# Performance work log

Measured on AMD Instinct MI355X. Metric: run time of the kernel, lower is better.

Reference implementation:

```python
import jax, jax.numpy as jnp
import numpy as np


def setup_inputs() -> dict:
    key = jax.random.key(0)
    ks = jax.random.split(key, 6)
    B, T, U = 4, 160, 80
    De, Dd = 640, 640
    inner, vocab = 640, 1024
    return {
        "enc_state": jax.random.normal(ks[0], (B, T, De), jnp.float32),
        "dec_state": jax.random.normal(ks[1], (B, U, Dd), jnp.float32),
        "W1": jax.random.normal(ks[2], (De + Dd, inner), jnp.float32) * (1.0 / np.sqrt(De + Dd)),
        "b1": jax.random.normal(ks[3], (inner,), jnp.float32) * 0.02,
        "W2": jax.random.normal(ks[4], (inner, vocab), jnp.float32) * (1.0 / np.sqrt(inner)),
        "b2": jax.random.normal(ks[5], (vocab,), jnp.float32) * 0.02,
    }


def reference(enc_state, dec_state, W1, b1, W2, b2):
    # Faithful to: cat([enc tiled over U, dec tiled over T], -1) @ W1 + b1,
    # algebraically split so the [B,T,U,2D] concat is never materialized:
    # cat(e, d) @ W1 == e @ W1[:De] + d @ W1[De:]
    De = enc_state.shape[-1]
    W1_enc, W1_dec = W1[:De], W1[De:]
    enc_proj = jnp.einsum("btd,dh->bth", enc_state, W1_enc)   # [B,T,H]
    dec_proj = jnp.einsum("bud,dh->buh", dec_state, W1_dec)   # [B,U,H]
    # broadcast add over the (T,U) lattice -> [B,T,U,H]
    hidden = jnp.tanh(enc_proj[:, :, None, :] + dec_proj[:, None, :, :] + b1)
    logits = jnp.einsum("btuh,hv->btuv", hidden, W2) + b2     # [B,T,U,V]
    return logits
```

## Files before the change

### kernel.cpp

```cpp
#include <hip/hip_runtime.h>
#include <hip/hip_bf16.h>
#include <cstdint>

#define B_    4
#define T_    160
#define U_    80
#define D_    640
#define V_    1024
#define BT_   640
#define BU_   320
#define M_    51200

typedef __bf16 bf16x8 __attribute__((ext_vector_type(8)));
typedef float floatx4 __attribute__((ext_vector_type(4)));

__device__ __forceinline__ void g2l16(const void* g, void* l) {
    __builtin_amdgcn_global_load_lds((const __attribute__((address_space(1))) void*)g,
                                     (__attribute__((address_space(3))) void*)l,
                                     16, 0, 0);
}

__device__ __forceinline__ float fast_tanh(float x) {
    float e = __builtin_amdgcn_exp2f(x * 2.8853900817779268f);
    return 1.0f - 2.0f * __builtin_amdgcn_rcpf(e + 1.0f);
}

__global__ __launch_bounds__(256) void proj_kernel(
    const float* __restrict__ enc, const float* __restrict__ dec,
    const float* __restrict__ W1,
    float* __restrict__ encp, float* __restrict__ decp) {
    __shared__ float As[32][36];
    __shared__ float Ws[32][36];

    const int rt = blockIdx.y;
    const int ct = blockIdx.x;
    const float* Asrc;
    const float* Wsrc;
    float* Cdst;
    if (rt < 20) { Asrc = enc + (size_t)rt * 32 * D_;        Wsrc = W1;             Cdst = encp + (size_t)rt * 32 * D_; }
    else         { Asrc = dec + (size_t)(rt - 20) * 32 * D_; Wsrc = W1 + D_ * D_;   Cdst = decp + (size_t)(rt - 20) * 32 * D_; }

    const int tid = threadIdx.x;
    const int ar = tid >> 3, ac = (tid & 7) * 4;
    const int tr = tid >> 4, tc = tid & 15;

    float a00 = 0.f, a01 = 0.f, a10 = 0.f, a11 = 0.f;
    for (int k0 = 0; k0 < D_; k0 += 32) {
        __syncthreads();
        *(floatx4*)&As[ar][ac] = *(const floatx4*)&Asrc[(size_t)ar * D_ + k0 + ac];
        *(floatx4*)&Ws[ar][ac] = *(const floatx4*)&Wsrc[(size_t)(k0 + ar) * D_ + ct * 32 + ac];
        __syncthreads();
#pragma unroll
        for (int kk = 0; kk < 32; kk++) {
            float x0 = As[tr * 2][kk], x1 = As[tr * 2 + 1][kk];
            float w0 = Ws[kk][tc * 2], w1 = Ws[kk][tc * 2 + 1];
            a00 += x0 * w0; a01 += x0 * w1;
            a10 += x1 * w0; a11 += x1 * w1;
        }
    }
    const int cc = ct * 32 + tc * 2;
    Cdst[(size_t)(tr * 2) * D_ + cc]     = a00;
    Cdst[(size_t)(tr * 2) * D_ + cc + 1] = a01;
    Cdst[(size_t)(tr * 2 + 1) * D_ + cc]     = a10;
    Cdst[(size_t)(tr * 2 + 1) * D_ + cc + 1] = a11;
}

__global__ __launch_bounds__(256) void w2t_kernel(
    const float* __restrict__ W2, __bf16* __restrict__ W2t) {
    __shared__ __bf16 tile[32][33];
    const int vt = blockIdx.x;
    const int kt = blockIdx.y;
    const int tx = threadIdx.x & 31, ty = threadIdx.x >> 5;
#pragma unroll
    for (int i = 0; i < 4; i++)
        tile[ty + i * 8][tx] = (__bf16)W2[(size_t)(kt * 32 + ty + i * 8) * V_ + vt * 32 + tx];
    __syncthreads();
#pragma unroll
    for (int i = 0; i < 4; i++)
        W2t[(size_t)(vt * 32 + ty + i * 8) * D_ + kt * 32 + tx] = tile[tx][ty + i * 8];
}

__global__ __launch_bounds__(256) void hidden_kernel(
    const float* __restrict__ encp, const float* __restrict__ decp,
    const float* __restrict__ b1, __bf16* __restrict__ H) {
    const unsigned g = blockIdx.x * 256u + threadIdx.x;
    const unsigned row = g / 80u;
    const unsigned hg  = g % 80u;
    const unsigned u   = row % 80u;
    const unsigned bt  = row / 80u;
    const unsigned b   = bt / 160u;

    const float* ep = encp + (size_t)bt * D_ + hg * 8;
    const float* dp = decp + (size_t)(b * 80u + u) * D_ + hg * 8;
    const float* bp = b1 + hg * 8;

    floatx4 e0 = *(const floatx4*)ep,       e1 = *(const floatx4*)(ep + 4);
    floatx4 d0 = *(const floatx4*)dp,       d1 = *(const floatx4*)(dp + 4);
    floatx4 c0 = *(const floatx4*)bp,       c1 = *(const floatx4*)(bp + 4);

    bf16x8 hv;
#pragma unroll
    for (int i = 0; i < 4; i++) hv[i]     = (__bf16)fast_tanh(e0[i] + d0[i] + c0[i]);
#pragma unroll
    for (int i = 0; i < 4; i++) hv[i + 4] = (__bf16)fast_tanh(e1[i] + d1[i] + c1[i]);

    *(bf16x8*)(H + (size_t)g * 8) = hv;
}

#define VM4  asm volatile("s_waitcnt vmcnt(4)" ::: "memory")
#define VM0  asm volatile("s_waitcnt vmcnt(0)" ::: "memory")
#define BAR  __builtin_amdgcn_s_barrier()
#define SCB  __builtin_amdgcn_sched_barrier(0)

#define STG_A(BUF, S, TL) do { \
    g2l16(Hb + (unsigned)((S)*163840 + (TL)*128) + agl,         ldsp + (BUF)*32768 + (S)*16384 + stl); \
    g2l16(Hb + (unsigned)((S)*163840 + (TL)*128 + 10240) + agl, ldsp + (BUF)*32768 + (S)*16384 + stl + 1024); \
  } while (0)
#define STG_B(BUF, S, TL) do { \
    g2l16(Wb + (unsigned)((S)*163840 + (TL)*128) + agl,         ldsp + 65536 + (BUF)*32768 + (S)*16384 + stl); \
    g2l16(Wb + (unsigned)((S)*163840 + (TL)*128 + 10240) + agl, ldsp + 65536 + (BUF)*32768 + (S)*16384 + stl + 1024); \
  } while (0)

#define PHASE(QM, QN, ABUF, BBUF, STAGE_STMT, WAIT_STMT) do { \
    bf16x8 af0[4], af1[4], bg0[2], bg1[2]; \
    _Pragma("unroll") for (int ii = 0; ii < 4; ++ii) { \
      af0[ii] = *(const bf16x8*)(ldsp + (ABUF)*32768 + (QM)*16384 + ii*2048 + aRowB + sx0); \
      af1[ii] = *(const bf16x8*)(ldsp + (ABUF)*32768 + (QM)*16384 + ii*2048 + aRowB + sx1); \
    } \
    _Pragma("unroll") for (int jj = 0; jj < 2; ++jj) { \
      bg0[jj] = *(const bf16x8*)(ldsp + 65536 + (BBUF)*32768 + (QN)*16384 + jj*2048 + bRowB + sx0); \
      bg1[jj] = *(const bf16x8*)(ldsp + 65536 + (BBUF)*32768 + (QN)*16384 + jj*2048 + bRowB + sx1); \
    } \
    STAGE_STMT; \
    WAIT_STMT; \
    BAR; SCB; \
    __builtin_amdgcn_s_setprio(1); \
    _Pragma("unroll") for (int ii = 0; ii < 4; ++ii) \
      _Pragma("unroll") for (int jj = 0; jj < 2; ++jj) { \
        acc[(QM)*4+ii][(QN)*2+jj] = __builtin_amdgcn_mfma_f32_16x16x32_bf16(af0[ii], bg0[jj], acc[(QM)*4+ii][(QN)*2+jj], 0, 0, 0); \
        acc[(QM)*4+ii][(QN)*2+jj] = __builtin_amdgcn_mfma_f32_16x16x32_bf16(af1[ii], bg1[jj], acc[(QM)*4+ii][(QN)*2+jj], 0, 0, 0); \
      } \
    __builtin_amdgcn_s_setprio(0); \
    BAR; SCB; \
  } while (0)

__global__ __launch_bounds__(512, 2) void gemm_kernel(
    const __bf16* __restrict__ H, const __bf16* __restrict__ W2t,
    const float* __restrict__ b2, float* __restrict__ C) {
    __shared__ __align__(128) char lds[131072];

    const int bid = blockIdx.x;
    const int swz = (bid & 7) * 100 + (bid >> 3);
    const int mt = swz >> 2, nt = swz & 3;
    const int m0 = mt * 256, n0 = nt * 256;

    const int tid = threadIdx.x;
    const int w = tid >> 6, l = tid & 63;
    const int wr = w >> 2, wc = w & 3;
    const int lrow = l & 15, lk = l >> 4, l7 = l & 7, lhi = l >> 3;

    const unsigned swzb = (unsigned)(((l & 7) ^ lhi) * 16);
    const unsigned agl  = (unsigned)((w * 16 + lhi) * 1280) + swzb;
    const unsigned stl  = (unsigned)(w * 2048 + l * 16);

    const char* Hb = (const char*)H   + (size_t)m0 * 1280;
    const char* Wb = (const char*)W2t + (size_t)n0 * 1280;
    char* ldsp = (char*)lds;

    const unsigned aRowB = (unsigned)((wr * 64 + lrow) * 128);
    const unsigned bRowB = (unsigned)(wc * 4096 + lrow * 128);
    const unsigned sx0 = (unsigned)(((0 + lk) ^ l7) * 16);
    const unsigned sx1 = (unsigned)(((4 + lk) ^ l7) * 16);

    floatx4 acc[8][4] = {};

    STG_A(0, 0, 0); STG_A(0, 1, 0); STG_B(0, 0, 0); STG_B(0, 1, 0);
    STG_A(1, 0, 1); STG_B(1, 0, 1);
    VM4; BAR; SCB;

#pragma unroll 1
    for (int it = 0; it < 5; ++it) {
        const int t1 = 2 * it + 1, t2 = 2 * it + 2, t3 = 2 * it + 3;
        const bool pf = (it < 4);
        PHASE(0, 0, 0, 0, { STG_A(1, 1, t1); STG_B(1, 1, t1); }, (void)0);
        PHASE(0, 1, 0, 0, (void)0, (void)0);
        PHASE(1, 0, 0, 0, { if (pf) STG_A(0, 0, t2); }, (void)0);
        PHASE(1, 1, 0, 0, { if (pf) STG_B(0, 0, t2); },
                          { if (it == 4) { VM0; } else { VM4; } });
        PHASE(0, 0, 1, 1, { if (pf) { STG_A(0, 1, t2); STG_B(0, 1, t2); } }, (void)0);
        PHASE(0, 1, 1, 1, (void)0, (void)0);
        PHASE(1, 0, 1, 1, { if (pf) STG_A(1, 0, t3); }, (void)0);
        PHASE(1, 1, 1, 1, { if (pf) STG_B(1, 0, t3); }, VM4);
    }

#pragma unroll
    for (int j = 0; j < 4; ++j) {
        const int col = n0 + (j >> 1) * 128 + wc * 32 + (j & 1) * 16 + lrow;
        const float bj = b2[col];
#pragma unroll
        for (int i = 0; i < 8; ++i) {
            const int row = m0 + (i >> 2) * 128 + wr * 64 + (i & 3) * 16 + lk * 4;
            float* Cp = C + (size_t)row * V_ + col;
#pragma unroll
            for (int rg = 0; rg < 4; ++rg)
                Cp[(size_t)rg * V_] = acc[i][j][rg] + bj;
        }
    }
}

extern "C" void kernel_launch(void* const* d_in, const int* in_sizes, int n_in,
                              void* d_out, int out_size, void* d_ws, size_t ws_size,
                              hipStream_t stream) {
    const float* enc = (const float*)d_in[0];
    const float* dec = (const float*)d_in[1];
    const float* W1  = (const float*)d_in[2];
    const float* b1  = (const float*)d_in[3];
    const float* W2  = (const float*)d_in[4];
    const float* b2  = (const float*)d_in[5];
    float* out = (float*)d_out;

    char* ws = (char*)d_ws;
    float*  encp = (float*)ws;
    float*  decp = (float*)(ws + 1638400);
    __bf16* W2t  = (__bf16*)(ws + 1638400 + 819200);
    __bf16* Hbuf = (__bf16*)(ws + 1638400 + 819200 + 1310720);

    proj_kernel<<<dim3(20, 30), 256, 0, stream>>>(enc, dec, W1, encp, decp);
    w2t_kernel<<<dim3(32, 20), 256, 0, stream>>>(W2, W2t);
    hidden_kernel<<<16000, 256, 0, stream>>>(encp, decp, b1, Hbuf);
    gemm_kernel<<<800, 512, 0, stream>>>(Hbuf, W2t, b2, out);
}
```

Baseline: 345.3 us.

## Reuse MFMA fragments across GEMM phases and enlarge projection tiles

The bf16 GEMM main loop now reads A and B fragments from LDS once and reuses them across neighbouring quadrant phases. A fragments are shared across the two N-quadrants and B fragments across the two M-quadrants, which cuts LDS read traffic per K-step. The fp32 projection kernel moves from 32x32 tiles with 2x2 per-thread outputs to 64x64 tiles with 4x4 register blocking and vectorised stores, raising arithmetic intensity. The cost is more live fragment registers in the GEMM, which could pressure occupancy at 512 threads and 2 blocks per CU. The projection launch also shrinks to 150 blocks, which may underfill the GPU.

```diff
diff --git a/kernel.cpp b/kernel.cpp
--- a/kernel.cpp
+++ b/kernel.cpp
@@ -29,40 +29,45 @@
     const float* __restrict__ enc, const float* __restrict__ dec,
     const float* __restrict__ W1,
     float* __restrict__ encp, float* __restrict__ decp) {
-    __shared__ float As[32][36];
-    __shared__ float Ws[32][36];
+    __shared__ float As[64][36];
+    __shared__ float Ws[32][68];
 
     const int rt = blockIdx.y;
     const int ct = blockIdx.x;
-    const float* Asrc;
-    const float* Wsrc;
-    float* Cdst;
-    if (rt < 20) { Asrc = enc + (size_t)rt * 32 * D_;        Wsrc = W1;             Cdst = encp + (size_t)rt * 32 * D_; }
-    else         { Asrc = dec + (size_t)(rt - 20) * 32 * D_; Wsrc = W1 + D_ * D_;   Cdst = decp + (size_t)(rt - 20) * 32 * D_; }
+    const float* Asrc; const float* Wsrc; float* Cdst;
+    if (rt < 10) { Asrc = enc + (size_t)rt * 64 * D_;        Wsrc = W1;           Cdst = encp + (size_t)rt * 64 * D_; }
+    else         { Asrc = dec + (size_t)(rt - 10) * 64 * D_; Wsrc = W1 + D_ * D_; Cdst = decp + (size_t)(rt - 10) * 64 * D_; }
 
     const int tid = threadIdx.x;
-    const int ar = tid >> 3, ac = (tid & 7) * 4;
-    const int tr = tid >> 4, tc = tid & 15;
-
-    float a00 = 0.f, a01 = 0.f, a10 = 0.f, a11 = 0.f;
+    const int ar = tid >> 2,  ac = (tid & 3) * 8;
+    const int wr2 = tid >> 3, wc2 = (tid & 7) * 8;
+    const int tr = tid >> 4,  tc = tid & 15;
+
+    float acc[4][4] = {};
     for (int k0 = 0; k0 < D_; k0 += 32) {
         __syncthreads();
-        *(floatx4*)&As[ar][ac] = *(const floatx4*)&Asrc[(size_t)ar * D_ + k0 + ac];
-        *(floatx4*)&Ws[ar][ac] = *(const floatx4*)&Wsrc[(size_t)(k0 + ar) * D_ + ct * 32 + ac];
+        *(floatx4*)&As[ar][ac]       = *(const floatx4*)&Asrc[(size_t)ar * D_ + k0 + ac];
+        *(floatx4*)&As[ar][ac + 4]   = *(const floatx4*)&Asrc[(size_t)ar * D_ + k0 + ac + 4];
+        *(floatx4*)&Ws[wr2][wc2]     = *(const floatx4*)&Wsrc[(size_t)(k0 + wr2) * D_ + ct * 64 + wc2];
+        *(floatx4*)&Ws[wr2][wc2 + 4] = *(const floatx4*)&Wsrc[(size_t)(k0 + wr2) * D_ + ct * 64 + wc2 + 4];
         __syncthreads();
 #pragma unroll
         for (int kk = 0; kk < 32; kk++) {
-            float x0 = As[tr * 2][kk], x1 = As[tr * 2 + 1][kk];
-            float w0 = Ws[kk][tc * 2], w1 = Ws[kk][tc * 2 + 1];
-            a00 += x0 * w0; a01 += x0 * w1;
-            a10 += x1 * w0; a11 += x1 * w1;
+            floatx4 w = *(const floatx4*)&Ws[kk][tc * 4];
+            float a0 = As[tr * 4 + 0][kk], a1 = As[tr * 4 + 1][kk];
+            float a2 = As[tr * 4 + 2][kk], a3 = As[tr * 4 + 3][kk];
+#pragma unroll
+            for (int j = 0; j < 4; j++) {
+                acc[0][j] += a0 * w[j]; acc[1][j] += a1 * w[j];
+                acc[2][j] += a2 * w[j]; acc[3][j] += a3 * w[j];
+            }
         }
     }
-    const int cc = ct * 32 + tc * 2;
-    Cdst[(size_t)(tr * 2) * D_ + cc]     = a00;
-    Cdst[(size_t)(tr * 2) * D_ + cc + 1] = a01;
-    Cdst[(size_t)(tr * 2 + 1) * D_ + cc]     = a10;
-    Cdst[(size_t)(tr * 2 + 1) * D_ + cc + 1] = a11;
+#pragma unroll
+    for (int i = 0; i < 4; i++) {
+        floatx4 v = { acc[i][0], acc[i][1], acc[i][2], acc[i][3] };
+        *(floatx4*)&Cdst[(size_t)(tr * 4 + i) * D_ + ct * 64 + tc * 4] = v;
+    }
 }
 
 __global__ __launch_bounds__(256) void w2t_kernel(
@@ -121,27 +126,24 @@
     g2l16(Wb + (unsigned)((S)*163840 + (TL)*128 + 10240) + agl, ldsp + 65536 + (BUF)*32768 + (S)*16384 + stl + 1024); \
   } while (0)
 
-#define PHASE(QM, QN, ABUF, BBUF, STAGE_STMT, WAIT_STMT) do { \
-    bf16x8 af0[4], af1[4], bg0[2], bg1[2]; \
+#define RD_A(ABUF, QM) do { \
     _Pragma("unroll") for (int ii = 0; ii < 4; ++ii) { \
       af0[ii] = *(const bf16x8*)(ldsp + (ABUF)*32768 + (QM)*16384 + ii*2048 + aRowB + sx0); \
       af1[ii] = *(const bf16x8*)(ldsp + (ABUF)*32768 + (QM)*16384 + ii*2048 + aRowB + sx1); \
-    } \
+    } } while (0)
+#define RD_B(BG0, BG1, BBUF, QN) do { \
     _Pragma("unroll") for (int jj = 0; jj < 2; ++jj) { \
-      bg0[jj] = *(const bf16x8*)(ldsp + 65536 + (BBUF)*32768 + (QN)*16384 + jj*2048 + bRowB + sx0); \
-      bg1[jj] = *(const bf16x8*)(ldsp + 65536 + (BBUF)*32768 + (QN)*16384 + jj*2048 + bRowB + sx1); \
-    } \
-    STAGE_STMT; \
-    WAIT_STMT; \
-    BAR; SCB; \
+      BG0[jj] = *(const bf16x8*)(ldsp + 65536 + (BBUF)*32768 + (QN)*16384 + jj*2048 + bRowB + sx0); \
+      BG1[jj] = *(const bf16x8*)(ldsp + 65536 + (BBUF)*32768 + (QN)*16384 + jj*2048 + bRowB + sx1); \
+    } } while (0)
+#define MM(QM, QN, BG0, BG1) do { \
     __builtin_amdgcn_s_setprio(1); \
     _Pragma("unroll") for (int ii = 0; ii < 4; ++ii) \
       _Pragma("unroll") for (int jj = 0; jj < 2; ++jj) { \
-        acc[(QM)*4+ii][(QN)*2+jj] = __builtin_amdgcn_mfma_f32_16x16x32_bf16(af0[ii], bg0[jj], acc[(QM)*4+ii][(QN)*2+jj], 0, 0, 0); \
-        acc[(QM)*4+ii][(QN)*2+jj] = __builtin_amdgcn_mfma_f32_16x16x32_bf16(af1[ii], bg1[jj], acc[(QM)*4+ii][(QN)*2+jj], 0, 0, 0); \
+        acc[(QM)*4+ii][(QN)*2+jj] = __builtin_amdgcn_mfma_f32_16x16x32_bf16(af0[ii], BG0[jj], acc[(QM)*4+ii][(QN)*2+jj], 0, 0, 0); \
+        acc[(QM)*4+ii][(QN)*2+jj] = __builtin_amdgcn_mfma_f32_16x16x32_bf16(af1[ii], BG1[jj], acc[(QM)*4+ii][(QN)*2+jj], 0, 0, 0); \
       } \
     __builtin_amdgcn_s_setprio(0); \
-    BAR; SCB; \
   } while (0)
 
 __global__ __launch_bounds__(512, 2) void gemm_kernel(
@@ -182,15 +184,31 @@
     for (int it = 0; it < 5; ++it) {
         const int t1 = 2 * it + 1, t2 = 2 * it + 2, t3 = 2 * it + 3;
         const bool pf = (it < 4);
-        PHASE(0, 0, 0, 0, { STG_A(1, 1, t1); STG_B(1, 1, t1); }, (void)0);
-        PHASE(0, 1, 0, 0, (void)0, (void)0);
-        PHASE(1, 0, 0, 0, { if (pf) STG_A(0, 0, t2); }, (void)0);
-        PHASE(1, 1, 0, 0, { if (pf) STG_B(0, 0, t2); },
-                          { if (it == 4) { VM0; } else { VM4; } });
-        PHASE(0, 0, 1, 1, { if (pf) { STG_A(0, 1, t2); STG_B(0, 1, t2); } }, (void)0);
-        PHASE(0, 1, 1, 1, (void)0, (void)0);
-        PHASE(1, 0, 1, 1, { if (pf) STG_A(1, 0, t3); }, (void)0);
-        PHASE(1, 1, 1, 1, { if (pf) STG_B(1, 0, t3); }, VM4);
+        bf16x8 af0[4], af1[4], bgA0[2], bgA1[2], bgB0[2], bgB1[2];
+
+        RD_A(0, 0); RD_B(bgA0, bgA1, 0, 0);
+        STG_A(1, 1, t1); STG_B(1, 1, t1);
+        BAR; SCB; MM(0, 0, bgA0, bgA1); BAR; SCB;
+        RD_B(bgB0, bgB1, 0, 1);
+        BAR; SCB; MM(0, 1, bgB0, bgB1); BAR; SCB;
+        RD_A(0, 1);
+        if (pf) STG_A(0, 0, t2);
+        BAR; SCB; MM(1, 0, bgA0, bgA1); BAR; SCB;
+        if (pf) STG_B(0, 0, t2);
+        if (it == 4) { VM0; } else { VM4; }
+        BAR; SCB; MM(1, 1, bgB0, bgB1); BAR; SCB;
+
+        RD_A(1, 0); RD_B(bgA0, bgA1, 1, 0);
+        if (pf) { STG_A(0, 1, t2); STG_B(0, 1, t2); }
+        BAR; SCB; MM(0, 0, bgA0, bgA1); BAR; SCB;
+        RD_B(bgB0, bgB1, 1, 1);
+        BAR; SCB; MM(0, 1, bgB0, bgB1); BAR; SCB;
+        RD_A(1, 1);
+        if (pf) STG_A(1, 0, t3);
+        BAR; SCB; MM(1, 0, bgA0, bgA1); BAR; SCB;
+        if (pf) STG_B(1, 0, t3);
+        VM4;
+        BAR; SCB; MM(1, 1, bgB0, bgB1); BAR; SCB;
     }
 
 #pragma unroll
@@ -225,7 +243,7 @@
     __bf16* W2t  = (__bf16*)(ws + 1638400 + 819200);
     __bf16* Hbuf = (__bf16*)(ws + 1638400 + 819200 + 1310720);
 
-    proj_kernel<<<dim3(20, 30), 256, 0, stream>>>(enc, dec, W1, encp, decp);
+    proj_kernel<<<dim3(10, 15), 256, 0, stream>>>(enc, dec, W1, encp, decp);
     w2t_kernel<<<dim3(32, 20), 256, 0, stream>>>(W2, W2t);
     hidden_kernel<<<16000, 256, 0, stream>>>(encp, decp, b1, Hbuf);
     gemm_kernel<<<800, 512, 0, stream>>>(Hbuf, W2t, b2, out);
```

Measured after the change: 355.9 us. +3.1%, slower.
